# Kernel tuning notes

Measured on AMD Instinct MI355X. Metric: run time of the kernel, lower is better.

## Reference

```python
import jax, jax.numpy as jnp
import numpy as np

GAMMA = 0.001

N_TEST, N_TRAIN, D, OUT = 8192, 8192, 512, 16

def setup_inputs() -> dict:
    key = jax.random.key(0)
    k1, k2, k3 = jax.random.split(key, 3)
    X = jax.random.normal(k1, (N_TEST, D), dtype=jnp.float32)
    train_X = jax.random.normal(k2, (N_TRAIN, D), dtype=jnp.float32)
    alpha = jax.random.normal(k3, (N_TRAIN, OUT), dtype=jnp.float32)
    return {"X": X, "train_X": train_X, "alpha": alpha}


def reference(X, train_X, alpha):
    # (same math as (x[:,None]-y[None])**2 summed over d, without the n*m*d blowup)
    x_sq = jnp.sum(X * X, axis=-1, keepdims=True)            # [n_test, 1]
    y_sq = jnp.sum(train_X * train_X, axis=-1)[None, :]       # [1, n_train]
    cross = X @ train_X.T                                     # [n_test, n_train]
    sq = x_sq + y_sq - 2.0 * cross
    K_test = jnp.exp(-GAMMA * sq)
    return K_test @ alpha                                     # [n_test, out]
```

## Files before the change

### kernel.cpp

```cpp
#include <hip/hip_runtime.h>
#include <stdint.h>

#define NROW 8192
#define DIM  512
#define NOUT 16
#define GAMMA 0.001f
#define EXP2S (2.0f * GAMMA * 1.44269504088896340736f)
#define SC1 0x7F7F7F7F

typedef __bf16 bf16_t;
typedef bf16_t bf16x4_t __attribute__((ext_vector_type(4)));
typedef bf16_t bf16x8_t __attribute__((ext_vector_type(8)));
typedef float  floatx4_t __attribute__((ext_vector_type(4)));
typedef int    intx4_t  __attribute__((ext_vector_type(4)));
typedef int    intx8_t  __attribute__((ext_vector_type(8)));

__device__ __forceinline__ void async_copy16(const void* g, const void* l) {
    __builtin_amdgcn_global_load_lds(
        (__attribute__((address_space(1))) void*)(uintptr_t)g,
        (__attribute__((address_space(3))) void*)(uint32_t)(uintptr_t)l,
        16, 0, 0);
}

__global__ __launch_bounds__(256) void prep_convert(
    const float* __restrict__ X, const float* __restrict__ T,
    const float* __restrict__ alpha,
    uint8_t* __restrict__ Xf, uint8_t* __restrict__ Tf,
    float* __restrict__ xfac, bf16_t* __restrict__ alphaTp)
{
    const int w = threadIdx.x >> 6, lane = threadIdx.x & 63;
    const int row = blockIdx.x * 4 + w;
    const bool is_test = row < NROW;
    const float* src = is_test ? X : T;
    uint8_t* dst = is_test ? Xf : Tf;
    const int r = is_test ? row : row - NROW;
    const float4* s4 = (const float4*)(src + (size_t)r * DIM);
    const float4 v0 = s4[lane * 2];
    const float4 v1 = s4[lane * 2 + 1];
    float ss = v0.x*v0.x + v0.y*v0.y + v0.z*v0.z + v0.w*v0.w
             + v1.x*v1.x + v1.y*v1.y + v1.z*v1.z + v1.w*v1.w;
    int lo = __builtin_amdgcn_cvt_pk_fp8_f32(v0.x, v0.y, 0, false);
    lo     = __builtin_amdgcn_cvt_pk_fp8_f32(v0.z, v0.w, lo, true);
    int hi = __builtin_amdgcn_cvt_pk_fp8_f32(v1.x, v1.y, 0, false);
    hi     = __builtin_amdgcn_cvt_pk_fp8_f32(v1.z, v1.w, hi, true);
    *(int2*)(dst + (size_t)r * DIM + lane * 8) = make_int2(lo, hi);
#pragma unroll
    for (int m = 32; m > 0; m >>= 1) ss += __shfl_xor(ss, m, 64);
    const float f = __expf(-GAMMA * ss);
    if (is_test) {
        if (lane == 0) xfac[r] = f;
    } else if (lane < 16) {
        alphaTp[(size_t)lane * NROW + r] = (bf16_t)(alpha[r * 16 + lane] * f);
    }
}

#define TPT 4
#define KLD2 72

__global__ __launch_bounds__(256, 2) void rbf_main(
    const uint8_t* __restrict__ Xf, const uint8_t* __restrict__ Tf,
    const bf16_t* __restrict__ alphaTp, const float* __restrict__ xfac,
    float* __restrict__ out)
{
    __shared__ __align__(16) unsigned char smem[36864];

    const int tid = threadIdx.x;
    const int w = tid >> 6, lane = tid & 63;
    const int wm = w >> 1, wn = w & 1;
    const int quad = lane >> 4, l15 = lane & 15;

    const int rb = blockIdx.x;
    const int chunk = blockIdx.y;
    const int row0 = rb * 128;
    const int cb0 = chunk * (TPT * 128);

    const int s_row = tid >> 3;
    const int s_ub = (((tid & 7) ^ (s_row & 7)) * 16);
    const uint8_t* gTp = Tf + (size_t)(cb0 + s_row) * DIM + s_ub;
    const unsigned ldsW = (unsigned)(w << 10);

    const int sw = l15 & 7;

    intx8_t xg[4][4];
#pragma unroll
    for (int g = 0; g < 4; ++g)
#pragma unroll
        for (int i = 0; i < 4; ++i)
            xg[g][i] = *(const intx8_t*)(Xf
                + (size_t)(row0 + wn * 64 + i * 16 + l15) * DIM
                + g * 128 + quad * 32);

    const floatx4_t vzero = {0.f, 0.f, 0.f, 0.f};
    floatx4_t oacc[4];
#pragma unroll
    for (int i = 0; i < 4; ++i) oacc[i] = vzero;

    bf16_t* kw = (bf16_t*)smem + w * (64 * KLD2);

    for (int t = 0; t < TPT; ++t) {
        const uint8_t* gTt = gTp + (size_t)(cb0 ? 0 : 0) + (size_t)t * 128 * DIM;

        floatx4_t acc[4][4];
#pragma unroll
        for (int i = 0; i < 4; ++i)
#pragma unroll
            for (int j = 0; j < 4; ++j) acc[i][j] = vzero;

        __syncthreads();
#pragma unroll
        for (int i = 0; i < 4; ++i)
            async_copy16(gTt + (size_t)i * 16384, smem + i * 4096 + ldsW);

#pragma unroll
        for (int g = 0; g < 4; ++g) {
            __syncthreads();
            if (g < 3) {
                const unsigned bb = ((g + 1) & 1) * 16384u;
                const int kb = (g + 1) * 128;
#pragma unroll
                for (int i = 0; i < 4; ++i)
                    async_copy16(gTt + (size_t)i * 16384 + kb, smem + bb + i * 4096 + ldsW);
            }
            const unsigned char* bufc = smem + (g & 1) * 16384;
#pragma unroll
            for (int mi = 0; mi < 4; ++mi) {
                const int rA = wm * 64 + mi * 16 + l15;
                const intx4_t alo = *(const intx4_t*)(bufc + rA * 128 + (((2 * quad) ^ sw) * 16));
                const intx4_t ahi = *(const intx4_t*)(bufc + rA * 128 + (((2 * quad + 1) ^ sw) * 16));
                const intx8_t ta = __builtin_shufflevector(alo, ahi, 0, 1, 2, 3, 4, 5, 6, 7);
#pragma unroll
                for (int ni = 0; ni < 4; ++ni)
                    acc[mi][ni] = __builtin_amdgcn_mfma_scale_f32_16x16x128_f8f6f4(
                        ta, xg[g][ni], acc[mi][ni], 0, 0, 0, SC1, 0, SC1);
            }
        }

        __syncthreads();
#pragma unroll
        for (int ni = 0; ni < 4; ++ni)
#pragma unroll
            for (int mi = 0; mi < 4; ++mi) {
                bf16x4_t pk;
#pragma unroll
                for (int r = 0; r < 4; ++r)
                    pk[r] = (bf16_t)__builtin_amdgcn_exp2f(acc[mi][ni][r] * EXP2S);
                *(bf16x4_t*)(kw + (ni * 16 + l15) * KLD2 + mi * 16 + quad * 4) = pk;
            }

        const int cb = cb0 + t * 128;
#pragma unroll
        for (int ks = 0; ks < 2; ++ks) {
            const bf16x8_t bv = *(const bf16x8_t*)(alphaTp + (size_t)l15 * NROW
                                                   + cb + wm * 64 + ks * 32 + quad * 8);
#pragma unroll
            for (int ni = 0; ni < 4; ++ni) {
                const bf16x8_t av = *(const bf16x8_t*)(kw + (ni * 16 + l15) * KLD2
                                                       + ks * 32 + quad * 8);
                oacc[ni] = __builtin_amdgcn_mfma_f32_16x16x32_bf16(av, bv, oacc[ni], 0, 0, 0);
            }
        }
    }

    __syncthreads();
    float* stash = (float*)smem;
    if (wm == 1) {
#pragma unroll
        for (int ni = 0; ni < 4; ++ni)
            *(floatx4_t*)(stash + wn * 1024 + ni * 256 + lane * 4) = oacc[ni];
    }
    __syncthreads();
    if (wm == 0) {
#pragma unroll
        for (int ni = 0; ni < 4; ++ni) {
            const floatx4_t o2 = *(const floatx4_t*)(stash + wn * 1024 + ni * 256 + lane * 4);
            const int trow = row0 + wn * 64 + ni * 16 + quad * 4;
            const float4 xf = *(const float4*)(xfac + trow);
            atomicAdd(out + (size_t)(trow + 0) * NOUT + l15, (oacc[ni][0] + o2[0]) * xf.x);
            atomicAdd(out + (size_t)(trow + 1) * NOUT + l15, (oacc[ni][1] + o2[1]) * xf.y);
            atomicAdd(out + (size_t)(trow + 2) * NOUT + l15, (oacc[ni][2] + o2[2]) * xf.z);
            atomicAdd(out + (size_t)(trow + 3) * NOUT + l15, (oacc[ni][3] + o2[3]) * xf.w);
        }
    }
}

extern "C" void kernel_launch(void* const* d_in, const int* in_sizes, int n_in,
                              void* d_out, int out_size, void* d_ws, size_t ws_size,
                              hipStream_t stream) {
    (void)in_sizes; (void)n_in; (void)out_size; (void)ws_size;
    const float* X     = (const float*)d_in[0];
    const float* T     = (const float*)d_in[1];
    const float* alpha = (const float*)d_in[2];

    char* ws = (char*)d_ws;
    uint8_t* Xf     = (uint8_t*)ws;
    uint8_t* Tf     = (uint8_t*)(ws + (8u << 20));
    float*   xfac   = (float*)(ws + (16u << 20));
    bf16_t*  alphaTp= (bf16_t*)(ws + (16u << 20) + (64u << 10));
    float*   out    = (float*)d_out;

    hipMemsetAsync(out, 0, (size_t)NROW * NOUT * sizeof(float), stream);
    prep_convert<<<4096, 256, 0, stream>>>(X, T, alpha, Xf, Tf, xfac, alphaTp);
    dim3 grid(64, 16);
    rbf_main<<<grid, 256, 0, stream>>>(Xf, Tf, alphaTp, xfac, out);
}
```

Baseline: 136.7 us.

## Pre-tile FP8 operands into MFMA-fragment layout and prefetch next tile across epilogue

The prep kernel now writes X and train_X in blocked 16-row tiles that match the MFMA fragment order. Register loads of X become contiguous and LDS reads of T need no XOR swizzle. The K-tile staging area is separated from the exp/bf16 scratch area, which grows LDS use, so the first chunk of the next T tile can be issued during the exp and second-GEMM epilogue and one barrier is dropped. Occupancy is pinned with waves_per_eu, at the cost of more LDS per block, which may limit residency.

Result: faster. 133.5 us (-2.4%).

```diff
diff --git a/kernel.cpp b/kernel.cpp
--- a/kernel.cpp
+++ b/kernel.cpp
@@ -32,7 +32,6 @@
     const int row = blockIdx.x * 4 + w;
     const bool is_test = row < NROW;
     const float* src = is_test ? X : T;
-    uint8_t* dst = is_test ? Xf : Tf;
     const int r = is_test ? row : row - NROW;
     const float4* s4 = (const float4*)(src + (size_t)r * DIM);
     const float4 v0 = s4[lane * 2];
@@ -43,7 +42,17 @@
     lo     = __builtin_amdgcn_cvt_pk_fp8_f32(v0.z, v0.w, lo, true);
     int hi = __builtin_amdgcn_cvt_pk_fp8_f32(v1.x, v1.y, 0, false);
     hi     = __builtin_amdgcn_cvt_pk_fp8_f32(v1.z, v1.w, hi, true);
-    *(int2*)(dst + (size_t)r * DIM + lane * 8) = make_int2(lo, hi);
+    size_t off;
+    if (is_test) {
+        off = (size_t)(r >> 4) * 8192 + ((lane >> 4) * 2048)
+            + (((lane >> 2) & 3) * 512) + ((r & 15) * 32) + ((lane & 3) * 8);
+        *(int2*)(Xf + off) = make_int2(lo, hi);
+    } else {
+        off = (size_t)(r >> 4) * 8192 + ((lane >> 4) * 2048)
+            + (((lane >> 1) & 1) * 1024) + (((lane >> 2) & 3) * 256)
+            + ((r & 15) * 16) + ((lane & 1) * 8);
+        *(int2*)(Tf + off) = make_int2(lo, hi);
+    }
 #pragma unroll
     for (int m = 32; m > 0; m >>= 1) ss += __shfl_xor(ss, m, 64);
     const float f = __expf(-GAMMA * ss);
@@ -57,12 +66,14 @@
 #define TPT 4
 #define KLD2 72
 
-__global__ __launch_bounds__(256, 2) void rbf_main(
+__global__ __launch_bounds__(256)
+__attribute__((amdgpu_waves_per_eu(2, 2)))
+void rbf_main(
     const uint8_t* __restrict__ Xf, const uint8_t* __restrict__ Tf,
     const bf16_t* __restrict__ alphaTp, const float* __restrict__ xfac,
     float* __restrict__ out)
 {
-    __shared__ __align__(16) unsigned char smem[36864];
+    __shared__ __align__(16) unsigned char smem[69632];
 
     const int tid = threadIdx.x;
     const int w = tid >> 6, lane = tid & 63;
@@ -74,59 +85,65 @@
     const int row0 = rb * 128;
     const int cb0 = chunk * (TPT * 128);
 
-    const int s_row = tid >> 3;
-    const int s_ub = (((tid & 7) ^ (s_row & 7)) * 16);
-    const uint8_t* gTp = Tf + (size_t)(cb0 + s_row) * DIM + s_ub;
-    const unsigned ldsW = (unsigned)(w << 10);
-
-    const int sw = l15 & 7;
-
+    const uint8_t* xbase = Xf + (size_t)((row0 >> 4) + wn * 4) * 8192
+                              + quad * 512 + l15 * 32;
     intx8_t xg[4][4];
 #pragma unroll
     for (int g = 0; g < 4; ++g)
 #pragma unroll
         for (int i = 0; i < 4; ++i)
-            xg[g][i] = *(const intx8_t*)(Xf
-                + (size_t)(row0 + wn * 64 + i * 16 + l15) * DIM
-                + g * 128 + quad * 32);
+            xg[g][i] = *(const intx8_t*)(xbase + (size_t)i * 8192 + g * 2048);
+#pragma unroll
+    for (int g = 0; g < 4; ++g)
+#pragma unroll
+        for (int i = 0; i < 4; ++i)
+            asm volatile("" : "+v"(xg[g][i]));
+
+    const uint8_t* gT0 = Tf + (size_t)((cb0 >> 4) + 2 * w) * 8192 + lane * 16;
+    const unsigned ldsT = (unsigned)(2 * w * 2048);
 
     const floatx4_t vzero = {0.f, 0.f, 0.f, 0.f};
     floatx4_t oacc[4];
 #pragma unroll
     for (int i = 0; i < 4; ++i) oacc[i] = vzero;
 
-    bf16_t* kw = (bf16_t*)smem + w * (64 * KLD2);
-
+    bf16_t* kw = (bf16_t*)(smem + 32768 + w * 9216);
+
+#pragma unroll
+    for (int sj = 0; sj < 2; ++sj)
+#pragma unroll
+        for (int j1 = 0; j1 < 2; ++j1)
+            async_copy16(gT0 + (size_t)sj * 8192 + j1 * 1024,
+                         smem + ldsT + sj * 2048 + j1 * 1024);
+
+#pragma unroll 1
     for (int t = 0; t < TPT; ++t) {
-        const uint8_t* gTt = gTp + (size_t)(cb0 ? 0 : 0) + (size_t)t * 128 * DIM;
-
         floatx4_t acc[4][4];
 #pragma unroll
         for (int i = 0; i < 4; ++i)
 #pragma unroll
             for (int j = 0; j < 4; ++j) acc[i][j] = vzero;
-
-        __syncthreads();
-#pragma unroll
-        for (int i = 0; i < 4; ++i)
-            async_copy16(gTt + (size_t)i * 16384, smem + i * 4096 + ldsW);
 
 #pragma unroll
         for (int g = 0; g < 4; ++g) {
             __syncthreads();
             if (g < 3) {
                 const unsigned bb = ((g + 1) & 1) * 16384u;
-                const int kb = (g + 1) * 128;
-#pragma unroll
-                for (int i = 0; i < 4; ++i)
-                    async_copy16(gTt + (size_t)i * 16384 + kb, smem + bb + i * 4096 + ldsW);
+                const size_t gofs = (size_t)t * 8 * 8192 + (g + 1) * 2048;
+#pragma unroll
+                for (int sj = 0; sj < 2; ++sj)
+#pragma unroll
+                    for (int j1 = 0; j1 < 2; ++j1)
+                        async_copy16(gT0 + gofs + (size_t)sj * 8192 + j1 * 1024,
+                                     smem + bb + ldsT + sj * 2048 + j1 * 1024);
             }
             const unsigned char* bufc = smem + (g & 1) * 16384;
 #pragma unroll
             for (int mi = 0; mi < 4; ++mi) {
-                const int rA = wm * 64 + mi * 16 + l15;
-                const intx4_t alo = *(const intx4_t*)(bufc + rA * 128 + (((2 * quad) ^ sw) * 16));
-                const intx4_t ahi = *(const intx4_t*)(bufc + rA * 128 + (((2 * quad + 1) ^ sw) * 16));
+                const unsigned char* sb = bufc + (wm * 4 + mi) * 2048
+                                        + quad * 256 + l15 * 16;
+                const intx4_t alo = *(const intx4_t*)(sb);
+                const intx4_t ahi = *(const intx4_t*)(sb + 1024);
                 const intx8_t ta = __builtin_shufflevector(alo, ahi, 0, 1, 2, 3, 4, 5, 6, 7);
 #pragma unroll
                 for (int ni = 0; ni < 4; ++ni)
@@ -135,7 +152,6 @@
             }
         }
 
-        __syncthreads();
 #pragma unroll
         for (int ni = 0; ni < 4; ++ni)
 #pragma unroll
@@ -159,6 +175,16 @@
                 oacc[ni] = __builtin_amdgcn_mfma_f32_16x16x32_bf16(av, bv, oacc[ni], 0, 0, 0);
             }
         }
+
+        if (t + 1 < TPT) {
+            const size_t gofs = (size_t)(t + 1) * 8 * 8192;
+#pragma unroll
+            for (int sj = 0; sj < 2; ++sj)
+#pragma unroll
+                for (int j1 = 0; j1 < 2; ++j1)
+                    async_copy16(gT0 + gofs + (size_t)sj * 8192 + j1 * 1024,
+                                 smem + ldsT + sj * 2048 + j1 * 1024);
+        }
     }
 
     __syncthreads();
@@ -166,13 +192,13 @@
     if (wm == 1) {
 #pragma unroll
         for (int ni = 0; ni < 4; ++ni)
-            *(floatx4_t*)(stash + wn * 1024 + ni * 256 + lane * 4) = oacc[ni];
+            *(floatx4_t*)(stash + (wn * 4 + ni) * 256 + lane * 4) = oacc[ni];
     }
     __syncthreads();
     if (wm == 0) {
 #pragma unroll
         for (int ni = 0; ni < 4; ++ni) {
-            const floatx4_t o2 = *(const floatx4_t*)(stash + wn * 1024 + ni * 256 + lane * 4);
+            const floatx4_t o2 = *(const floatx4_t*)(stash + (wn * 4 + ni) * 256 + lane * 4);
             const int trow = row0 + wn * 64 + ni * 16 + quad * 4;
             const float4 xf = *(const float4*)(xfac + trow);
             atomicAdd(out + (size_t)(trow + 0) * NOUT + l15, (oacc[ni][0] + o2[0]) * xf.x);
```
